# Kernel tuning notes

Hardware: AMD Instinct MI355X
Metric: run time of the kernel (lower is better)

Reference implementation:

```python
import jax, jax.numpy as jnp
import numpy as np

B, T, D = 2, 4096, 512
H = 8
HS = D // H  # 64
CTX = 4096


def setup_inputs() -> dict:
    key = jax.random.key(0)
    ks = jax.random.split(key, 10)
    s = lambda fan_in: fan_in ** -0.5
    x = jax.random.normal(ks[0], (B, T, D), dtype=jnp.float32)
    # per-head q/k/v projections (no bias), stacked over heads: [H, D, HS]
    Wq = jax.random.normal(ks[1], (H, D, HS), dtype=jnp.float32) * s(D)
    Wk = jax.random.normal(ks[2], (H, D, HS), dtype=jnp.float32) * s(D)
    Wv = jax.random.normal(ks[3], (H, D, HS), dtype=jnp.float32) * s(D)
    # output projection [D, D] + bias
    Wproj = jax.random.normal(ks[4], (D, D), dtype=jnp.float32) * s(D)
    bproj = jax.random.normal(ks[5], (D,), dtype=jnp.float32) * 0.01
    # feed-forward: D -> 4D -> D
    W1 = jax.random.normal(ks[6], (D, 4 * D), dtype=jnp.float32) * s(D)
    b1 = jax.random.normal(ks[7], (4 * D,), dtype=jnp.float32) * 0.01
    W2 = jax.random.normal(ks[8], (4 * D, D), dtype=jnp.float32) * s(4 * D)
    b2 = jax.random.normal(ks[9], (D,), dtype=jnp.float32) * 0.01
    return {"x": x, "Wq": Wq, "Wk": Wk, "Wv": Wv, "Wproj": Wproj,
            "bproj": bproj, "W1": W1, "b1": b1, "W2": W2, "b2": b2}


def reference(x, Wq, Wk, Wv, Wproj, bproj, W1, b1, W2, b2):
    Bx, Tx, Dx = x.shape
    scale = HS ** -0.5
    # multi-head causal self-attention (naive, full TxT scores as in source)
    q = jnp.einsum('btd,hde->bhte', x, Wq)
    k = jnp.einsum('btd,hde->bhte', x, Wk)
    v = jnp.einsum('btd,hde->bhte', x, Wv)
    wei = jnp.einsum('bhte,bhse->bhts', q, k) * scale  # [B,H,T,T]
    causal = jnp.tril(jnp.ones((Tx, Tx), dtype=bool))
    wei = jnp.where(causal, wei, -jnp.inf)
    wei = jax.nn.softmax(wei, axis=-1)
    attn = jnp.einsum('bhts,bhse->bhte', wei, v)  # [B,H,T,HS]
    # concat heads (cat along last dim == transpose+reshape of stacked heads)
    attn = attn.transpose(0, 2, 1, 3).reshape(Bx, Tx, Dx)
    sa_out = attn @ Wproj + bproj
    x = x + sa_out
    # feed-forward with residual
    h = jax.nn.relu(x @ W1 + b1)
    x = x + (h @ W2 + b2)
    return x
```

## Files before the change

kernel.cpp:

```cpp
#include <hip/hip_runtime.h>


typedef __attribute__((ext_vector_type(8))) short bf16x8;
typedef __attribute__((ext_vector_type(4))) float f32x4;
typedef __attribute__((ext_vector_type(16))) float f32x16;
typedef unsigned short u16;

__device__ __forceinline__ u16 f2bf(float f) {
  union { float f; unsigned int i; } u; u.f = f;
  unsigned int r = u.i + 0x7fffu + ((u.i >> 16) & 1u);
  return (u16)(r >> 16);
}
__device__ __forceinline__ float bf2f(u16 s) {
  union { unsigned int i; float f; } u; u.i = ((unsigned int)s) << 16;
  return u.f;
}
__device__ __forceinline__ void gload16(const void* g, void* l) {
  __builtin_amdgcn_global_load_lds((const __attribute__((address_space(1))) void*)g,
                                   (__attribute__((address_space(3))) void*)l,
                                   16, 0, 0);
}

__device__ __forceinline__ void plswap_u(unsigned &a, unsigned &b) {
#if defined(__has_builtin) && __has_builtin(__builtin_amdgcn_permlane32_swap)
  auto r = __builtin_amdgcn_permlane32_swap(a, b, false, false);
  a = (unsigned)r[0]; b = (unsigned)r[1];
#else
  asm("v_permlane32_swap_b32 %0, %1" : "+v"(a), "+v"(b));
#endif
}
__device__ __forceinline__ void plswap_f(float &a, float &b) {
  unsigned ua = __builtin_bit_cast(unsigned, a), ub = __builtin_bit_cast(unsigned, b);
  plswap_u(ua, ub);
  a = __builtin_bit_cast(float, ua); b = __builtin_bit_cast(float, ub);
}

__device__ __forceinline__ float tmax16(const f32x16 v) {
  float a = fmaxf(v[0], v[8]),  b = fmaxf(v[1], v[9]);
  float c = fmaxf(v[2], v[10]), d = fmaxf(v[3], v[11]);
  float e = fmaxf(v[4], v[12]), f = fmaxf(v[5], v[13]);
  float g = fmaxf(v[6], v[14]), h = fmaxf(v[7], v[15]);
  a = fmaxf(a, e); b = fmaxf(b, f); c = fmaxf(c, g); d = fmaxf(d, h);
  a = fmaxf(a, c); b = fmaxf(b, d);
  return fmaxf(a, b);
}
__device__ __forceinline__ float tsum16(const f32x16 v) {
  float a = v[0] + v[8],  b = v[1] + v[9];
  float c = v[2] + v[10], d = v[3] + v[11];
  float e = v[4] + v[12], f = v[5] + v[13];
  float g = v[6] + v[14], h = v[7] + v[15];
  a += e; b += f; c += g; d += h;
  a += c; b += d;
  return a + b;
}

__global__ void cast_x_kernel(const float4* __restrict__ in, ushort4* __restrict__ out, int n4) {
  int i = blockIdx.x * blockDim.x + threadIdx.x;
  if (i >= n4) return;
  float4 v = in[i];
  ushort4 o; o.x = f2bf(v.x); o.y = f2bf(v.y); o.z = f2bf(v.z); o.w = f2bf(v.w);
  out[i] = o;
}

__global__ void transpose_cast_kernel(const float* __restrict__ in, u16* __restrict__ out,
                                      int C, int ldo, long in_z, long out_z) {
  __shared__ float t[32][33];
  in += (long)blockIdx.z * in_z;
  out += (long)blockIdx.z * out_z;
  int c0 = blockIdx.x * 32, r0 = blockIdx.y * 32;
  int tx = threadIdx.x & 31, ty = threadIdx.x >> 5;
#pragma unroll
  for (int k = 0; k < 4; k++)
    t[ty + 8 * k][tx] = in[(long)(r0 + ty + 8 * k) * C + c0 + tx];
  __syncthreads();
#pragma unroll
  for (int k = 0; k < 4; k++)
    out[(long)(c0 + ty + 8 * k) * ldo + r0 + tx] = f2bf(t[tx][ty + 8 * k]);
}

__global__ void transpose_v_kernel(const u16* __restrict__ qkv, u16* __restrict__ vt) {
  __shared__ u16 t[32][33];
  int z = blockIdx.z;
  const u16* in = qkv + (long)(z >> 3) * 4096 * 1536 + 1024 + (z & 7) * 64;
  u16* out = vt + (long)z * 64 * 4096;
  int c0 = blockIdx.x * 32, r0 = blockIdx.y * 32;
  int tx = threadIdx.x & 31, ty = threadIdx.x >> 5;
#pragma unroll
  for (int k = 0; k < 4; k++)
    t[ty + 8 * k][tx] = in[(long)(r0 + ty + 8 * k) * 1536 + c0 + tx];
  __syncthreads();
#pragma unroll
  for (int k = 0; k < 4; k++)
    out[(long)(c0 + ty + 8 * k) * 4096 + r0 + tx] = t[tx][ty + 8 * k];
}

template <int MODE, int BN>
__global__ __launch_bounds__(256) void gemm_bt_kernel(
    const u16* __restrict__ A, const u16* __restrict__ Bt, void* __restrict__ Out,
    const float* __restrict__ bias, const float* __restrict__ resf,
    const u16* __restrict__ resb, int N, int K) {
  __shared__ __align__(16) char As[128 * 128];
  __shared__ __align__(16) char Bs[BN * 128];
  const int tid = threadIdx.x;
  const int lane = tid & 63, w = tid >> 6;
  const int l15 = lane & 15, l4 = lane >> 4;
  const long m0 = (long)blockIdx.y * 128;
  const long n0 = (long)blockIdx.x * BN;
  const int wm = (w >> 1) * 64, wn = (w & 1) * (BN / 2);
  const int NB = BN / 32;

  f32x4 acc[4][NB] = {};

  for (int kt = 0; kt < K; kt += 64) {
#pragma unroll
    for (int i = 0; i < 4; i++) {
      int basechunk = i * 256 + w * 64;
      int chunk = basechunk + lane;
      int row = chunk >> 3, c = chunk & 7;
      int sc = c ^ (row & 7);
      gload16(A + (m0 + row) * K + kt + sc * 8, As + basechunk * 16);
    }
#pragma unroll
    for (int i = 0; i < BN / 32; i++) {
      int basechunk = i * 256 + w * 64;
      int chunk = basechunk + lane;
      int row = chunk >> 3, c = chunk & 7;
      int sc = c ^ (row & 7);
      gload16(Bt + (n0 + row) * K + kt + sc * 8, Bs + basechunk * 16);
    }
    __syncthreads();
#pragma unroll
    for (int kk = 0; kk < 2; kk++) {
      bf16x8 a[4], b[NB];
#pragma unroll
      for (int m = 0; m < 4; m++) {
        int row = wm + m * 16 + l15;
        int ch = (kk * 4 + l4) ^ (row & 7);
        a[m] = *(const bf16x8*)(As + row * 128 + ch * 16);
      }
#pragma unroll
      for (int n = 0; n < NB; n++) {
        int row = wn + n * 16 + l15;
        int ch = (kk * 4 + l4) ^ (row & 7);
        b[n] = *(const bf16x8*)(Bs + row * 128 + ch * 16);
      }
#pragma unroll
      for (int m = 0; m < 4; m++)
#pragma unroll
        for (int n = 0; n < NB; n++)
          acc[m][n] = __builtin_amdgcn_mfma_f32_16x16x32_bf16(a[m], b[n], acc[m][n], 0, 0, 0);
    }
    __syncthreads();
  }

#pragma unroll
  for (int m = 0; m < 4; m++) {
#pragma unroll
    for (int n = 0; n < NB; n++) {
      long gcol = n0 + wn + n * 16 + l15;
#pragma unroll
      for (int r = 0; r < 4; r++) {
        long grow = m0 + wm + m * 16 + l4 * 4 + r;
        float v = acc[m][n][r];
        if (MODE == 0) {
          ((u16*)Out)[grow * N + gcol] = f2bf(v);
        } else if (MODE == 1) {
          v += bias[gcol] + resf[grow * N + gcol];
          ((u16*)Out)[grow * N + gcol] = f2bf(v);
        } else if (MODE == 2) {
          v += bias[gcol];
          v = v > 0.f ? v : 0.f;
          ((u16*)Out)[grow * N + gcol] = f2bf(v);
        } else {
          v += bias[gcol] + bf2f(resb[grow * N + gcol]);
          ((float*)Out)[grow * N + gcol] = v;
        }
      }
    }
  }
}

__global__ __launch_bounds__(256, 2) void attn_kernel(
    const u16* __restrict__ qkv, const u16* __restrict__ vt,
    float* __restrict__ pacc, float* __restrict__ pml) {
  __shared__ __align__(16) char Ks[2][64 * 128];
  __shared__ __align__(16) char Vs[2][64 * 128];
  const int tid = threadIdx.x;
  const int lane = tid & 63, w = tid >> 6;
  const int l31 = lane & 31, l5 = lane >> 5;
  const float cexp = 0.18033688f;

  const int g = blockIdx.x;
  const int bh = g & 15, b = bh >> 3, h = bh & 7;
  const u16* qbase = qkv + (long)b * 4096 * 1536 + h * 64;
  const u16* kbase = qbase + 512;
  const u16* vtbase = vt + (long)bh * 64 * 4096;

  for (int it = 0; it < 2; ++it) {
    const int qt = it ? 31 - (g >> 4) : (g >> 4);
    const int half = it;
    const int qt0 = qt * 128;
    const int j0 = half ? qt + 1 : 0;
    const int j1 = half ? 2 * qt + 2 : qt + 1;
    const int jdiag = 2 * qt;

    const int qrow_g = qt0 + w * 32 + l31;
    bf16x8 aq[4];
    {
      const u16* qp = qbase + (long)qrow_g * 1536 + l5 * 8;
#pragma unroll
      for (int kk = 0; kk < 4; kk++) aq[kk] = *(const bf16x8*)(qp + kk * 16);
    }

#pragma unroll
    for (int i = 0; i < 2; i++) {
      int basechunk = i * 256 + w * 64;
      int chunk = basechunk + lane;
      int row = chunk >> 3, c = chunk & 7;
      int sc = c ^ (row & 7);
      gload16(kbase + (long)(j0 * 64 + row) * 1536 + sc * 8, Ks[0] + basechunk * 16);
      gload16(vtbase + (long)row * 4096 + j0 * 64 + sc * 8, Vs[0] + basechunk * 16);
    }
    __syncthreads();

    f32x16 oacc[2] = {};
    float mi = -1e30f, li = 0.f;

    for (int j = j0; j < j1; ++j) {
      const int cur = (j - j0) & 1;
      if (j + 1 < j1) {
#pragma unroll
        for (int i = 0; i < 2; i++) {
          int basechunk = i * 256 + w * 64;
          int chunk = basechunk + lane;
          int row = chunk >> 3, c = chunk & 7;
          int sc = c ^ (row & 7);
          gload16(kbase + (long)((j + 1) * 64 + row) * 1536 + sc * 8, Ks[cur ^ 1] + basechunk * 16);
          gload16(vtbase + (long)row * 4096 + (j + 1) * 64 + sc * 8, Vs[cur ^ 1] + basechunk * 16);
        }
      }

      f32x16 st[2] = {};
      __builtin_amdgcn_s_setprio(1);
#pragma unroll
      for (int kk = 0; kk < 4; kk++) {
        int ch = ((l5 + 2 * kk) ^ (l31 & 7)) * 16;
        bf16x8 ak0 = *(const bf16x8*)(Ks[cur] + l31 * 128 + ch);
        bf16x8 ak1 = *(const bf16x8*)(Ks[cur] + (32 + l31) * 128 + ch);
        st[0] = __builtin_amdgcn_mfma_f32_32x32x16_bf16(ak0, aq[kk], st[0], 0, 0, 0);
        st[1] = __builtin_amdgcn_mfma_f32_32x32x16_bf16(ak1, aq[kk], st[1], 0, 0, 0);
      }
      __builtin_amdgcn_s_setprio(0);

      if (j >= jdiag) {
        int thr = qrow_g - j * 64;
#pragma unroll
        for (int n = 0; n < 2; n++)
#pragma unroll
          for (int reg = 0; reg < 16; reg++) {
            int key = n * 32 + 4 * l5 + (reg & 3) + 8 * (reg >> 2);
            if (key > thr) st[n][reg] = -1e30f;
          }
      }

      float pm = fmaxf(tmax16(st[0]), tmax16(st[1]));
      {
        float ta = pm, tb = pm;
        plswap_f(ta, tb);
        pm = fmaxf(ta, tb);
      }
      if (__any(pm > mi + 44.3614f)) {
        float mn = fmaxf(mi, pm);
        float alpha = exp2f((mi - mn) * cexp);
        mi = mn;
        li *= alpha;
#pragma unroll
        for (int ne = 0; ne < 2; ne++)
#pragma unroll
          for (int reg = 0; reg < 16; reg++) oacc[ne][reg] *= alpha;
      }
#pragma unroll
      for (int n = 0; n < 2; n++)
#pragma unroll
        for (int reg = 0; reg < 16; reg++)
          st[n][reg] = exp2f((st[n][reg] - mi) * cexp);
      float ps = tsum16(st[0]) + tsum16(st[1]);
      {
        float ta = ps, tb = ps;
        plswap_f(ta, tb);
        ps = ta + tb;
      }
      li += ps;

      unsigned bfr[4][4];
#pragma unroll
      for (int n = 0; n < 2; n++)
#pragma unroll
        for (int jj = 0; jj < 2; jj++)
#pragma unroll
          for (int t2 = 0; t2 < 2; t2++) {
            float lo0 = st[n][(2 * jj) * 4 + 2 * t2], hi0 = st[n][(2 * jj) * 4 + 2 * t2 + 1];
            float lo1 = st[n][(2 * jj + 1) * 4 + 2 * t2], hi1 = st[n][(2 * jj + 1) * 4 + 2 * t2 + 1];
            unsigned pa, pb;
            asm("v_cvt_pk_bf16_f32 %0, %1, %2" : "=v"(pa) : "v"(lo0), "v"(hi0));
            asm("v_cvt_pk_bf16_f32 %0, %1, %2" : "=v"(pb) : "v"(lo1), "v"(hi1));
            plswap_u(pa, pb);
            bfr[2 * n + jj][t2] = pa;
            bfr[2 * n + jj][2 + t2] = pb;
          }

      __builtin_amdgcn_s_setprio(1);
#pragma unroll
      for (int s = 0; s < 4; s++) {
        union { unsigned u[4]; bf16x8 v; } bp;
#pragma unroll
        for (int tt = 0; tt < 4; tt++) bp.u[tt] = bfr[s][tt];
        int ch = ((l5 + 2 * s) ^ (l31 & 7)) * 16;
        bf16x8 av0 = *(const bf16x8*)(Vs[cur] + l31 * 128 + ch);
        bf16x8 av1 = *(const bf16x8*)(Vs[cur] + (32 + l31) * 128 + ch);
        oacc[0] = __builtin_amdgcn_mfma_f32_32x32x16_bf16(av0, bp.v, oacc[0], 0, 0, 0);
        oacc[1] = __builtin_amdgcn_mfma_f32_32x32x16_bf16(av1, bp.v, oacc[1], 0, 0, 0);
      }
      __builtin_amdgcn_s_setprio(0);
      __syncthreads();
    }

    const int pidx = (bh * 32 + qt) * 2 + half;
    float* pa = pacc + (long)pidx * 8192;
#pragma unroll
    for (int ne = 0; ne < 2; ne++)
#pragma unroll
      for (int gg = 0; gg < 4; gg++) {
        float4 vv;
        vv.x = oacc[ne][4 * gg + 0];
        vv.y = oacc[ne][4 * gg + 1];
        vv.z = oacc[ne][4 * gg + 2];
        vv.w = oacc[ne][4 * gg + 3];
        *(float4*)(pa + (w * 32 + l31) * 64 + ne * 32 + 4 * l5 + 8 * gg) = vv;
      }
    if (l5 == 0) {
      float2 vv; vv.x = mi; vv.y = li;
      ((float2*)(pml + (long)pidx * 256))[w * 32 + l31] = vv;
    }
  }
}

__global__ __launch_bounds__(256) void attn_merge_kernel(
    const float* __restrict__ pacc, const float* __restrict__ pml, u16* __restrict__ attnb) {
  int tile = blockIdx.x;
  int bh = tile >> 5, qt = tile & 31;
  int b = bh >> 3, h = bh & 7;
  const float* a0 = pacc + (long)tile * 2 * 8192;
  const float* a1 = a0 + 8192;
  const float2* ml0 = (const float2*)(pml + (long)tile * 2 * 256);
  const float2* ml1 = ml0 + 128;
  int t = threadIdx.x;
  int cg = (t & 15) * 4;
  int rsub = t >> 4;
#pragma unroll
  for (int pass = 0; pass < 8; ++pass) {
    int row = pass * 16 + rsub;
    float2 v0 = ml0[row], v1 = ml1[row];
    float M = fmaxf(v0.x, v1.x);
    float w0 = __expf((v0.x - M) * 0.125f);
    float w1 = __expf((v1.x - M) * 0.125f);
    float inv = 1.f / (v0.y * w0 + v1.y * w1);
    float4 x0 = *(const float4*)(a0 + row * 64 + cg);
    float4 x1 = *(const float4*)(a1 + row * 64 + cg);
    ushort4 o;
    o.x = f2bf((x0.x * w0 + x1.x * w1) * inv);
    o.y = f2bf((x0.y * w0 + x1.y * w1) * inv);
    o.z = f2bf((x0.z * w0 + x1.z * w1) * inv);
    o.w = f2bf((x0.w * w0 + x1.w * w1) * inv);
    *(ushort4*)(attnb + ((long)(b * 4096 + qt * 128 + row)) * 512 + h * 64 + cg) = o;
  }
}

extern "C" void kernel_launch(void* const* d_in, const int* in_sizes, int n_in,
                              void* d_out, int out_size, void* d_ws, size_t ws_size,
                              hipStream_t stream) {
  const float* x = (const float*)d_in[0];
  const float* Wq = (const float*)d_in[1];
  const float* Wk = (const float*)d_in[2];
  const float* Wv = (const float*)d_in[3];
  const float* Wproj = (const float*)d_in[4];
  const float* bproj = (const float*)d_in[5];
  const float* W1 = (const float*)d_in[6];
  const float* b1 = (const float*)d_in[7];
  const float* W2 = (const float*)d_in[8];
  const float* b2 = (const float*)d_in[9];

  char* ws = (char*)d_ws;
  u16* xb      = (u16*)(ws);
  u16* wqkv_t  = (u16*)(ws + 8388608);
  u16* wproj_t = (u16*)(ws + 9961472);
  u16* w1_t    = (u16*)(ws + 10485760);
  u16* w2_t    = (u16*)(ws + 12582912);
  u16* qkv     = (u16*)(ws + 14680064);
  u16* vt      = (u16*)(ws + 39845888);
  u16* attnb   = (u16*)(ws + 48234496);
  u16* x1b     = (u16*)(ws + 56623104);
  u16* hbuf    = (u16*)(ws + 65011712);
  float* pml   = (float*)(ws + 56623104 + 2097152);
  float* pacc  = (float*)(ws + 65011712);

  cast_x_kernel<<<4096, 256, 0, stream>>>((const float4*)x, (ushort4*)xb, 8192 * 512 / 4);

  transpose_cast_kernel<<<dim3(2, 16, 8), 256, 0, stream>>>(Wq, wqkv_t, 64, 512, 32768L, 32768L);
  transpose_cast_kernel<<<dim3(2, 16, 8), 256, 0, stream>>>(Wk, wqkv_t + 512 * 512, 64, 512, 32768L, 32768L);
  transpose_cast_kernel<<<dim3(2, 16, 8), 256, 0, stream>>>(Wv, wqkv_t + 1024 * 512, 64, 512, 32768L, 32768L);
  transpose_cast_kernel<<<dim3(16, 16, 1), 256, 0, stream>>>(Wproj, wproj_t, 512, 512, 0, 0);
  transpose_cast_kernel<<<dim3(64, 16, 1), 256, 0, stream>>>(W1, w1_t, 2048, 512, 0, 0);
  transpose_cast_kernel<<<dim3(16, 64, 1), 256, 0, stream>>>(W2, w2_t, 512, 2048, 0, 0);

  gemm_bt_kernel<0, 128><<<dim3(12, 64), 256, 0, stream>>>(xb, wqkv_t, qkv, nullptr, nullptr, nullptr, 1536, 512);
  transpose_v_kernel<<<dim3(2, 128, 16), 256, 0, stream>>>(qkv, vt);
  attn_kernel<<<512, 256, 0, stream>>>(qkv, vt, pacc, pml);
  attn_merge_kernel<<<512, 256, 0, stream>>>(pacc, pml, attnb);
  gemm_bt_kernel<1, 64><<<dim3(8, 64), 256, 0, stream>>>(attnb, wproj_t, x1b, bproj, x, nullptr, 512, 512);
  gemm_bt_kernel<2, 128><<<dim3(16, 64), 256, 0, stream>>>(x1b, w1_t, hbuf, b1, nullptr, nullptr, 2048, 512);
  gemm_bt_kernel<3, 64><<<dim3(8, 64), 256, 0, stream>>>(hbuf, w2_t, d_out, b2, nullptr, x1b, 512, 2048);
}
```

Before: 221.9 us.

## Use 256-row query tiles with 4-way KV split and bf16 partials

The attention kernel now runs 512 threads (8 waves) per block and handles 256 query rows per tile. The key/value range is split into four equal chunks per tile, and work items are paired so that causal load stays balanced across the grid. Partial outputs are stored as bf16 instead of fp32, which halves partial-buffer traffic, and the merge kernel combines four partials per row. The larger Q tile lets each K/V load be reused by more rows, at the cost of a 4-way merge and some extra rounding in the partials.

```diff
diff --git a/kernel.cpp b/kernel.cpp
--- a/kernel.cpp
+++ b/kernel.cpp
@@ -180,9 +180,9 @@
   }
 }
 
-__global__ __launch_bounds__(256, 2) void attn_kernel(
+__global__ __launch_bounds__(512, 4) void attn_kernel(
     const u16* __restrict__ qkv, const u16* __restrict__ vt,
-    float* __restrict__ pacc, float* __restrict__ pml) {
+    u16* __restrict__ pacc, float* __restrict__ pml) {
   __shared__ __align__(16) char Ks[2][64 * 128];
   __shared__ __align__(16) char Vs[2][64 * 128];
   const int tid = threadIdx.x;
@@ -191,18 +191,20 @@
   const float cexp = 0.18033688f;
 
   const int g = blockIdx.x;
-  const int bh = g & 15, b = bh >> 3, h = bh & 7;
-  const u16* qbase = qkv + (long)b * 4096 * 1536 + h * 64;
-  const u16* kbase = qbase + 512;
-  const u16* vtbase = vt + (long)bh * 64 * 4096;
 
   for (int it = 0; it < 2; ++it) {
-    const int qt = it ? 31 - (g >> 4) : (g >> 4);
-    const int half = it;
-    const int qt0 = qt * 128;
-    const int j0 = half ? qt + 1 : 0;
-    const int j1 = half ? 2 * qt + 2 : qt + 1;
-    const int jdiag = 2 * qt;
+    const int item = it ? 1023 - g : g;
+    const int qt = item >> 6;
+    const int bh = (item >> 2) & 15;
+    const int qq = item & 3;
+    const int b = bh >> 3, h = bh & 7;
+    const int qt0 = qt * 256;
+    const int L = qt + 1;
+    const int j0 = qq * L, j1 = j0 + L;
+    const int jdiag = 4 * qt;
+    const u16* qbase = qkv + (long)b * 4096 * 1536 + h * 64;
+    const u16* kbase = qbase + 512;
+    const u16* vtbase = vt + (long)bh * 64 * 4096;
 
     const int qrow_g = qt0 + w * 32 + l31;
     bf16x8 aq[4];
@@ -212,14 +214,10 @@
       for (int kk = 0; kk < 4; kk++) aq[kk] = *(const bf16x8*)(qp + kk * 16);
     }
 
-#pragma unroll
-    for (int i = 0; i < 2; i++) {
-      int basechunk = i * 256 + w * 64;
-      int chunk = basechunk + lane;
-      int row = chunk >> 3, c = chunk & 7;
-      int sc = c ^ (row & 7);
-      gload16(kbase + (long)(j0 * 64 + row) * 1536 + sc * 8, Ks[0] + basechunk * 16);
-      gload16(vtbase + (long)row * 4096 + j0 * 64 + sc * 8, Vs[0] + basechunk * 16);
+    {
+      int row = tid >> 3, c = tid & 7, sc = c ^ (row & 7);
+      gload16(kbase + (long)(j0 * 64 + row) * 1536 + sc * 8, Ks[0] + w * 1024);
+      gload16(vtbase + (long)row * 4096 + j0 * 64 + sc * 8, Vs[0] + w * 1024);
     }
     __syncthreads();
 
@@ -229,15 +227,9 @@
     for (int j = j0; j < j1; ++j) {
       const int cur = (j - j0) & 1;
       if (j + 1 < j1) {
-#pragma unroll
-        for (int i = 0; i < 2; i++) {
-          int basechunk = i * 256 + w * 64;
-          int chunk = basechunk + lane;
-          int row = chunk >> 3, c = chunk & 7;
-          int sc = c ^ (row & 7);
-          gload16(kbase + (long)((j + 1) * 64 + row) * 1536 + sc * 8, Ks[cur ^ 1] + basechunk * 16);
-          gload16(vtbase + (long)row * 4096 + (j + 1) * 64 + sc * 8, Vs[cur ^ 1] + basechunk * 16);
-        }
+        int row = tid >> 3, c = tid & 7, sc = c ^ (row & 7);
+        gload16(kbase + (long)((j + 1) * 64 + row) * 1536 + sc * 8, Ks[cur ^ 1] + w * 1024);
+        gload16(vtbase + (long)row * 4096 + (j + 1) * 64 + sc * 8, Vs[cur ^ 1] + w * 1024);
       }
 
       f32x16 st[2] = {};
@@ -325,54 +317,67 @@
       __syncthreads();
     }
 
-    const int pidx = (bh * 32 + qt) * 2 + half;
-    float* pa = pacc + (long)pidx * 8192;
+    u16* pa = pacc + (long)item * 16384;
 #pragma unroll
     for (int ne = 0; ne < 2; ne++)
 #pragma unroll
       for (int gg = 0; gg < 4; gg++) {
-        float4 vv;
-        vv.x = oacc[ne][4 * gg + 0];
-        vv.y = oacc[ne][4 * gg + 1];
-        vv.z = oacc[ne][4 * gg + 2];
-        vv.w = oacc[ne][4 * gg + 3];
-        *(float4*)(pa + (w * 32 + l31) * 64 + ne * 32 + 4 * l5 + 8 * gg) = vv;
+        ushort4 o;
+        o.x = f2bf(oacc[ne][4 * gg + 0]);
+        o.y = f2bf(oacc[ne][4 * gg + 1]);
+        o.z = f2bf(oacc[ne][4 * gg + 2]);
+        o.w = f2bf(oacc[ne][4 * gg + 3]);
+        *(ushort4*)(pa + (w * 32 + l31) * 64 + ne * 32 + 4 * l5 + 8 * gg) = o;
       }
     if (l5 == 0) {
       float2 vv; vv.x = mi; vv.y = li;
-      ((float2*)(pml + (long)pidx * 256))[w * 32 + l31] = vv;
+      ((float2*)(pml + (long)item * 512))[w * 32 + l31] = vv;
     }
   }
 }
 
 __global__ __launch_bounds__(256) void attn_merge_kernel(
-    const float* __restrict__ pacc, const float* __restrict__ pml, u16* __restrict__ attnb) {
+    const u16* __restrict__ pacc, const float* __restrict__ pml, u16* __restrict__ attnb) {
+  const float cexp = 0.18033688f;
   int tile = blockIdx.x;
-  int bh = tile >> 5, qt = tile & 31;
+  int qt = tile >> 4, bh = tile & 15;
   int b = bh >> 3, h = bh & 7;
-  const float* a0 = pacc + (long)tile * 2 * 8192;
-  const float* a1 = a0 + 8192;
-  const float2* ml0 = (const float2*)(pml + (long)tile * 2 * 256);
-  const float2* ml1 = ml0 + 128;
+  int ibase = qt * 64 + bh * 4;
+  const u16* pq[4];
+  const float2* mlq[4];
+#pragma unroll
+  for (int q = 0; q < 4; q++) {
+    pq[q] = pacc + (long)(ibase + q) * 16384;
+    mlq[q] = (const float2*)(pml + (long)(ibase + q) * 512);
+  }
   int t = threadIdx.x;
   int cg = (t & 15) * 4;
   int rsub = t >> 4;
 #pragma unroll
-  for (int pass = 0; pass < 8; ++pass) {
+  for (int pass = 0; pass < 16; ++pass) {
     int row = pass * 16 + rsub;
-    float2 v0 = ml0[row], v1 = ml1[row];
-    float M = fmaxf(v0.x, v1.x);
-    float w0 = __expf((v0.x - M) * 0.125f);
-    float w1 = __expf((v1.x - M) * 0.125f);
-    float inv = 1.f / (v0.y * w0 + v1.y * w1);
-    float4 x0 = *(const float4*)(a0 + row * 64 + cg);
-    float4 x1 = *(const float4*)(a1 + row * 64 + cg);
+    float2 v[4];
+#pragma unroll
+    for (int q = 0; q < 4; q++) v[q] = mlq[q][row];
+    float M = fmaxf(fmaxf(v[0].x, v[1].x), fmaxf(v[2].x, v[3].x));
+    float acc0 = 0.f, acc1 = 0.f, acc2 = 0.f, acc3 = 0.f, denom = 0.f;
+#pragma unroll
+    for (int q = 0; q < 4; q++) {
+      float wq = exp2f((v[q].x - M) * cexp);
+      denom += v[q].y * wq;
+      ushort4 u = *(const ushort4*)(pq[q] + row * 64 + cg);
+      acc0 += wq * bf2f(u.x);
+      acc1 += wq * bf2f(u.y);
+      acc2 += wq * bf2f(u.z);
+      acc3 += wq * bf2f(u.w);
+    }
+    float inv = 1.f / denom;
     ushort4 o;
-    o.x = f2bf((x0.x * w0 + x1.x * w1) * inv);
-    o.y = f2bf((x0.y * w0 + x1.y * w1) * inv);
-    o.z = f2bf((x0.z * w0 + x1.z * w1) * inv);
-    o.w = f2bf((x0.w * w0 + x1.w * w1) * inv);
-    *(ushort4*)(attnb + ((long)(b * 4096 + qt * 128 + row)) * 512 + h * 64 + cg) = o;
+    o.x = f2bf(acc0 * inv);
+    o.y = f2bf(acc1 * inv);
+    o.z = f2bf(acc2 * inv);
+    o.w = f2bf(acc3 * inv);
+    *(ushort4*)(attnb + ((long)(b * 4096 + qt * 256 + row)) * 512 + h * 64 + cg) = o;
   }
 }
 
@@ -402,7 +407,7 @@
   u16* x1b     = (u16*)(ws + 56623104);
   u16* hbuf    = (u16*)(ws + 65011712);
   float* pml   = (float*)(ws + 56623104 + 2097152);
-  float* pacc  = (float*)(ws + 65011712);
+  u16* pacc    = (u16*)(ws + 65011712);
 
   cast_x_kernel<<<4096, 256, 0, stream>>>((const float4*)x, (ushort4*)xb, 8192 * 512 / 4);
 
@@ -415,8 +420,8 @@
 
   gemm_bt_kernel<0, 128><<<dim3(12, 64), 256, 0, stream>>>(xb, wqkv_t, qkv, nullptr, nullptr, nullptr, 1536, 512);
   transpose_v_kernel<<<dim3(2, 128, 16), 256, 0, stream>>>(qkv, vt);
-  attn_kernel<<<512, 256, 0, stream>>>(qkv, vt, pacc, pml);
-  attn_merge_kernel<<<512, 256, 0, stream>>>(pacc, pml, attnb);
+  attn_kernel<<<512, 512, 0, stream>>>(qkv, vt, pacc, pml);
+  attn_merge_kernel<<<256, 256, 0, stream>>>(pacc, pml, attnb);
   gemm_bt_kernel<1, 64><<<dim3(8, 64), 256, 0, stream>>>(attnb, wproj_t, x1b, bproj, x, nullptr, 512, 512);
   gemm_bt_kernel<2, 128><<<dim3(16, 64), 256, 0, stream>>>(x1b, w1_t, hbuf, b1, nullptr, nullptr, 2048, 512);
   gemm_bt_kernel<3, 64><<<dim3(8, 64), 256, 0, stream>>>(hbuf, w2_t, d_out, b2, nullptr, x1b, 512, 2048);
```

New measurement: 221.7 us. No clear change (-0.1%).
